# Kernel optimization log

Hardware: AMD Instinct MI355X
Metric: run time of the kernel (lower is better)

Reference implementation:

```python
import jax, jax.numpy as jnp
import numpy as np

D_MODEL = 1024
NUM_HEADS = 16
D_HEAD = D_MODEL // NUM_HEADS
BATCH = 2
SEQ = 2048


def setup_inputs() -> dict:
    key = jax.random.key(0)
    ks = jax.random.split(key, 5)
    std = 0.02
    return {
        "x": jax.random.normal(ks[0], (BATCH, SEQ, D_MODEL), dtype=jnp.float32),
        "Wq": jax.random.normal(ks[1], (D_MODEL, D_MODEL), dtype=jnp.float32) * std,
        "Wk": jax.random.normal(ks[2], (D_MODEL, D_MODEL), dtype=jnp.float32) * std,
        "Wv": jax.random.normal(ks[3], (D_MODEL, D_MODEL), dtype=jnp.float32) * std,
        "Wo": jax.random.normal(ks[4], (D_MODEL, D_MODEL), dtype=jnp.float32) * std,
    }


def reference(x, Wq, Wk, Wv, Wo):
    batch, seq_len, d_model = x.shape
    h, dh = NUM_HEADS, D_HEAD

    def split_heads(W):
        # x @ W.T -> (b, s, d) -> (b, h, s, dh)
        p = jnp.einsum('bsd,ed->bse', x, W)
        return p.reshape(batch, seq_len, h, dh).transpose(0, 2, 1, 3)

    Q = split_heads(Wq)
    K = split_heads(Wk)
    V = split_heads(Wv)

    scale = 1.0 / jnp.sqrt(jnp.asarray(dh, dtype=x.dtype))
    scores = jnp.einsum('bhqd,bhkd->bhqk', Q, K) * scale
    causal = jnp.tril(jnp.ones((seq_len, seq_len), dtype=bool))
    scores = jnp.where(causal, scores, -jnp.inf)
    attn = jax.nn.softmax(scores, axis=-1)
    out = jnp.einsum('bhqk,bhkd->bhqd', attn, V)  # (b, h, s, dh)
    out = out.transpose(0, 2, 1, 3).reshape(batch, seq_len, d_model)
    return jnp.einsum('bsd,ed->bse', out, Wo)
```

## Files before the change

kernel.cpp:

```cpp
#include <hip/hip_runtime.h>

#define D_MODEL 1024
#define NUM_HEADS 16
#define D_HEAD 64
#define BATCH 2
#define SEQ 2048
#define MTOT (BATCH * SEQ)
#define PLANE ((size_t)MTOT * D_MODEL)
#define QSCALE 0.1803368801f

typedef unsigned short us;
typedef __bf16 bf16x8 __attribute__((ext_vector_type(8)));
typedef float floatx4 __attribute__((ext_vector_type(4)));

__device__ __forceinline__ unsigned int f2bf(float f) {
  union { float f; unsigned int i; } v; v.f = f;
  unsigned int r = v.i + 0x7FFFu + ((v.i >> 16) & 1u);
  return r >> 16;
}
__device__ __forceinline__ unsigned int f2bf_tr(float f) {
  union { float f; unsigned int i; } v; v.f = f;
  return v.i >> 16;
}

__global__ __launch_bounds__(256) void convert_all(const float* __restrict__ x,
                                                   const float* __restrict__ Wq,
                                                   const float* __restrict__ Wk,
                                                   const float* __restrict__ Wv,
                                                   const float* __restrict__ Wo,
                                                   us* __restrict__ xbf,
                                                   us* __restrict__ Wqkv,
                                                   us* __restrict__ Wobf) {
  const int i = blockIdx.x * 256 + threadIdx.x;
  const float* src;
  us* dst;
  if (i < (1 << 20)) {
    src = x + (size_t)i * 4;
    dst = xbf + (size_t)i * 4;
  } else {
    const int j = i - (1 << 20);
    const int w = j >> 18;
    const int o = j & ((1 << 18) - 1);
    if (w < 3) {
      const float* ws = (w == 0) ? Wq : (w == 1) ? Wk : Wv;
      src = ws + (size_t)o * 4;
      dst = Wqkv + (size_t)w * (D_MODEL * D_MODEL) + (size_t)o * 4;
    } else {
      src = Wo + (size_t)o * 4;
      dst = Wobf + (size_t)o * 4;
    }
  }
  float4 v = *(const float4*)src;
  uint2 pk;
  pk.x = f2bf(v.x) | (f2bf(v.y) << 16);
  pk.y = f2bf(v.z) | (f2bf(v.w) << 16);
  *(uint2*)dst = pk;
}

template <int CMODE>
__global__ __launch_bounds__(256) void gemm_n64(const us* __restrict__ A,
                                                const us* __restrict__ B,
                                                void* __restrict__ Cv,
                                                int M, int N, int K) {
  __shared__ __bf16 As[2][128 * 32];
  __shared__ __bf16 Bs[2][64 * 32];
  const int tid = threadIdx.x;
  const int wid = tid >> 6;
  const int lane = tid & 63;
  const int bm = blockIdx.y * 128;
  const int bn = blockIdx.x * 64;
  const int wm = wid * 32;
  const int lr = lane & 15;
  const int quad = lane >> 4;

  floatx4 acc[2][4] = {};

  auto stage = [&](int buf, int k0) {
#pragma unroll
    for (int p = 0; p < 2; ++p) {
      const int cb = wid * 128 + p * 64;
      const int c = cb + lane;
      const us* ga = A + (size_t)(bm + (c >> 2)) * K + (k0 + (c & 3) * 8);
      __builtin_amdgcn_global_load_lds((const __attribute__((address_space(1))) void*)ga,
                                       (__attribute__((address_space(3))) void*)(&As[buf][cb * 8]),
                                       16, 0, 0);
    }
    const int cb2 = wid * 64;
    const int c2 = cb2 + lane;
    const us* gb = B + (size_t)(bn + (c2 >> 2)) * K + (k0 + (c2 & 3) * 8);
    __builtin_amdgcn_global_load_lds((const __attribute__((address_space(1))) void*)gb,
                                     (__attribute__((address_space(3))) void*)(&Bs[buf][cb2 * 8]),
                                     16, 0, 0);
  };

  stage(0, 0);
  __syncthreads();

  int cur = 0;
  for (int k0 = 0; k0 < K; k0 += 32) {
    if (k0 + 32 < K) stage(cur ^ 1, k0 + 32);

    bf16x8 a[2], b[4];
#pragma unroll
    for (int i = 0; i < 2; ++i)
      a[i] = *(const bf16x8*)&As[cur][(wm + i * 16 + lr) * 32 + quad * 8];
#pragma unroll
    for (int j = 0; j < 4; ++j)
      b[j] = *(const bf16x8*)&Bs[cur][(j * 16 + lr) * 32 + quad * 8];
#pragma unroll
    for (int i = 0; i < 2; ++i)
#pragma unroll
      for (int j = 0; j < 4; ++j)
        acc[i][j] = __builtin_amdgcn_mfma_f32_16x16x32_bf16(a[i], b[j], acc[i][j], 0, 0, 0);

    __syncthreads();
    cur ^= 1;
  }

#pragma unroll
  for (int i = 0; i < 2; ++i) {
#pragma unroll
    for (int j = 0; j < 4; ++j) {
      const int col = bn + j * 16 + lr;
      if constexpr (CMODE == 1) {
        us* dst = (us*)Cv;
        const int plane = col >> 10;
        if (plane < 2) {
          const float s = (plane == 0) ? QSCALE : 1.0f;
#pragma unroll
          for (int r = 0; r < 4; ++r) {
            const int row = bm + wm + i * 16 + quad * 4 + r;
            dst[(size_t)plane * PLANE + (size_t)row * 1024 + (col & 1023)] =
                (us)f2bf(acc[i][j][r] * s);
          }
        } else {
          const int d = col & 63;
          const int hh = (col >> 6) & 15;
          const int row0 = bm + wm + i * 16 + quad * 4;
          const int bb = row0 >> 11;
          const int ss = row0 & 2047;
          uint2 pk;
          pk.x = f2bf(acc[i][j][0]) | (f2bf(acc[i][j][1]) << 16);
          pk.y = f2bf(acc[i][j][2]) | (f2bf(acc[i][j][3]) << 16);
          *(uint2*)&dst[2 * PLANE + ((size_t)((bb * 16 + hh) * 64 + d)) * 2048 + ss] = pk;
        }
      } else {
#pragma unroll
        for (int r = 0; r < 4; ++r) {
          const int row = bm + wm + i * 16 + quad * 4 + r;
          ((float*)Cv)[(size_t)row * N + col] = acc[i][j][r];
        }
      }
    }
  }
}

#define ASTR 72

__global__ __launch_bounds__(512, 2) void attn_mfma(const us* __restrict__ Qb,
                                                    const us* __restrict__ Kb,
                                                    const us* __restrict__ Vtg,
                                                    us* __restrict__ Ob) {
  const int bx = blockIdx.x;
  const int b = bx >> 8;
  const int idx = bx & 255;
  const int h = idx >> 4;
  const int s0 = idx & 15;
  const int strip = b ? (15 - s0) : s0;
  const int q0 = strip * 128;
  const int ntiles = 2 * strip + 2;
  const int tid = threadIdx.x;
  const int w = tid >> 6;
  const int lane = tid & 63;
  const int lr = lane & 15;
  const int quad = lane >> 4;

  __shared__ us Ks[2][64 * ASTR];
  __shared__ us Vs[2][64 * ASTR];
  __shared__ us Ps[8 * 16 * ASTR];

  const us* kbase = Kb + (size_t)(b * SEQ) * D_MODEL + h * D_HEAD;
  const us* vbase = Vtg + (size_t)((b * 16 + h) * 64) * 2048;
  us* const pg = &Ps[w * 16 * ASTR];

  const int grow = q0 + w * 16;
  const us* qp = Qb + (size_t)(b * SEQ + grow + lr) * D_MODEL + h * D_HEAD;
  const bf16x8 qa0 = *(const bf16x8*)(qp + quad * 8);
  const bf16x8 qa1 = *(const bf16x8*)(qp + 32 + quad * 8);

  floatx4 oacc[4] = {};
  floatx4 lacc = {};
  bf16x8 ones;
#pragma unroll
  for (int i = 0; i < 8; ++i) ones[i] = (__bf16)1.0f;

  const int srow = tid >> 3;
  const int schunk = tid & 7;

  uint4 kreg, vreg;
  kreg = *(const uint4*)(kbase + (size_t)srow * D_MODEL + schunk * 8);
  vreg = *(const uint4*)(vbase + (size_t)srow * 2048 + schunk * 8);
  *(uint4*)&Ks[0][srow * ASTR + schunk * 8] = kreg;
  *(uint4*)&Vs[0][srow * ASTR + schunk * 8] = vreg;
  __syncthreads();

  for (int t = 0; t < ntiles; ++t) {
    const int k0 = t * 64;
    const int cur = t & 1;
    const bool more = (t + 1 < ntiles);

    if (more) {
      const int kn = k0 + 64;
      kreg = *(const uint4*)(kbase + (size_t)(kn + srow) * D_MODEL + schunk * 8);
      vreg = *(const uint4*)(vbase + (size_t)srow * 2048 + kn + schunk * 8);
    }

#pragma unroll
    for (int jt = 0; jt < 4; ++jt) {
      const bf16x8 kb0 = *(const bf16x8*)&Ks[cur][(jt * 16 + lr) * ASTR + quad * 8];
      const bf16x8 kb1 = *(const bf16x8*)&Ks[cur][(jt * 16 + lr) * ASTR + 32 + quad * 8];
      floatx4 s = {};
      s = __builtin_amdgcn_mfma_f32_16x16x32_bf16(kb0, qa0, s, 0, 0, 0);
      s = __builtin_amdgcn_mfma_f32_16x16x32_bf16(kb1, qa1, s, 0, 0, 0);
      const int kb = k0 + jt * 16 + quad * 4;
      const bool needMask = (k0 + jt * 16 + 15 > grow);
      float p[4];
#pragma unroll
      for (int r = 0; r < 4; ++r) {
        float e = __builtin_amdgcn_exp2f(s[r]);
        if (needMask && (kb + r > grow + lr)) e = 0.f;
        p[r] = e;
      }
      uint2 pk;
      pk.x = f2bf_tr(p[0]) | (f2bf_tr(p[1]) << 16);
      pk.y = f2bf_tr(p[2]) | (f2bf_tr(p[3]) << 16);
      *(uint2*)&pg[lr * ASTR + jt * 16 + quad * 4] = pk;
    }

    const bf16x8 pa0 = *(const bf16x8*)&pg[lr * ASTR + quad * 8];
    const bf16x8 pa1 = *(const bf16x8*)&pg[lr * ASTR + 32 + quad * 8];
    lacc = __builtin_amdgcn_mfma_f32_16x16x32_bf16(ones, pa0, lacc, 0, 0, 0);
    lacc = __builtin_amdgcn_mfma_f32_16x16x32_bf16(ones, pa1, lacc, 0, 0, 0);
#pragma unroll
    for (int nt = 0; nt < 4; ++nt) {
      const bf16x8 vb0 = *(const bf16x8*)&Vs[cur][(nt * 16 + lr) * ASTR + quad * 8];
      const bf16x8 vb1 = *(const bf16x8*)&Vs[cur][(nt * 16 + lr) * ASTR + 32 + quad * 8];
      oacc[nt] = __builtin_amdgcn_mfma_f32_16x16x32_bf16(vb0, pa0, oacc[nt], 0, 0, 0);
      oacc[nt] = __builtin_amdgcn_mfma_f32_16x16x32_bf16(vb1, pa1, oacc[nt], 0, 0, 0);
    }

    if (more) {
      const int nxt = cur ^ 1;
      *(uint4*)&Ks[nxt][srow * ASTR + schunk * 8] = kreg;
      *(uint4*)&Vs[nxt][srow * ASTR + schunk * 8] = vreg;
    }
    __syncthreads();
  }

  const float inv = 1.f / lacc[0];
#pragma unroll
  for (int nt = 0; nt < 4; ++nt) {
    uint2 pk;
    pk.x = f2bf_tr(oacc[nt][0] * inv) | (f2bf_tr(oacc[nt][1] * inv) << 16);
    pk.y = f2bf_tr(oacc[nt][2] * inv) | (f2bf_tr(oacc[nt][3] * inv) << 16);
    *(uint2*)&pg[lr * ASTR + nt * 16 + quad * 4] = pk;
  }
#pragma unroll
  for (int p = 0; p < 2; ++p) {
    const int c = lane + 64 * p;
    *(uint4*)(Ob + (size_t)(b * SEQ + grow + (c >> 3)) * D_MODEL + h * D_HEAD + (c & 7) * 8) =
        *(const uint4*)&pg[(c >> 3) * ASTR + (c & 7) * 8];
  }
}

extern "C" void kernel_launch(void* const* d_in, const int* in_sizes, int n_in,
                              void* d_out, int out_size, void* d_ws, size_t ws_size,
                              hipStream_t stream) {
  const float* x  = (const float*)d_in[0];
  const float* Wq = (const float*)d_in[1];
  const float* Wk = (const float*)d_in[2];
  const float* Wv = (const float*)d_in[3];
  const float* Wo = (const float*)d_in[4];

  us* xbf = (us*)d_ws;
  us* Qb  = xbf + PLANE;
  us* Kb  = xbf + 2 * PLANE;
  us* Vt  = xbf + 3 * PLANE;
  us* Wobf = xbf + 4 * PLANE;
  us* Ab  = xbf;
  us* Wqkv = (us*)d_out;
  float* out = (float*)d_out;

  convert_all<<<8192, 256, 0, stream>>>(x, Wq, Wk, Wv, Wo, xbf, Wqkv, Wobf);

  gemm_n64<1><<<dim3(3072 / 64, MTOT / 128), 256, 0, stream>>>(xbf, Wqkv, Qb, MTOT, 3072, D_MODEL);

  attn_mfma<<<512, 512, 0, stream>>>(Qb, Kb, Vt, Ab);

  gemm_n64<2><<<dim3(D_MODEL / 64, MTOT / 128), 256, 0, stream>>>(Ab, Wobf, out, MTOT, D_MODEL, D_MODEL);
}
```

Before: 185.7 us.

## Use 256x256-tile triple-buffered GEMM with direct-to-LDS loads for QKV projection

Replaces the 128x64-tile QKV projection GEMM with a new 512-thread kernel using 256x256 tiles. It adds a three-stage LDS pipeline fed by global_load_lds, an XOR swizzle to avoid bank conflicts, and setprio around the MFMA bursts. The larger tile raises arithmetic intensity and the asynchronous loads are meant to hide memory latency. The grid shrinks to 192 blocks, which may underfill the GPU's 256 CUs, and the kernel needs a large LDS footprint.

```diff
diff --git a/kernel.cpp b/kernel.cpp
--- a/kernel.cpp
+++ b/kernel.cpp
@@ -57,10 +57,135 @@
   *(uint2*)dst = pk;
 }
 
-template <int CMODE>
+__global__ __launch_bounds__(512) void gemm256(const us* __restrict__ A,
+                                               const us* __restrict__ B,
+                                               us* __restrict__ dst,
+                                               int K) {
+  __shared__ us As[3][256 * 32];
+  __shared__ us Bs[3][256 * 32];
+  const int tid = threadIdx.x;
+  const int wid = tid >> 6;
+  const int lane = tid & 63;
+  const int bm = blockIdx.y * 256;
+  const int bn = blockIdx.x * 256;
+  const int wm = (wid >> 2) * 128;
+  const int wn = (wid & 3) * 64;
+  const int lr = lane & 15;
+  const int quad = lane >> 4;
+  const int csel = (quad ^ ((lr >> 1) & 3)) * 8;
+
+  floatx4 acc[8][4] = {};
+
+  const int srow = tid >> 2;
+  const int sc = tid & 3;
+
+  auto stageA = [&](int buf, int k0, int p) {
+    const int row = srow + p * 128;
+    const int cs = (sc ^ ((row >> 1) & 3)) * 8;
+    const us* g = A + (size_t)(bm + row) * K + k0 + cs;
+    __builtin_amdgcn_global_load_lds((const __attribute__((address_space(1))) void*)g,
+                                     (__attribute__((address_space(3))) void*)(&As[buf][row * 32 + sc * 8]),
+                                     16, 0, 0);
+  };
+  auto stageB = [&](int buf, int k0, int p) {
+    const int row = srow + p * 128;
+    const int cs = (sc ^ ((row >> 1) & 3)) * 8;
+    const us* g = B + (size_t)(bn + row) * K + k0 + cs;
+    __builtin_amdgcn_global_load_lds((const __attribute__((address_space(1))) void*)g,
+                                     (__attribute__((address_space(3))) void*)(&Bs[buf][row * 32 + sc * 8]),
+                                     16, 0, 0);
+  };
+
+#pragma unroll
+  for (int p = 0; p < 2; ++p) { stageA(0, 0, p); stageB(0, 0, p); }
+#pragma unroll
+  for (int p = 0; p < 2; ++p) { stageA(1, 32, p); stageB(1, 32, p); }
+  asm volatile("s_waitcnt vmcnt(4)" ::: "memory");
+  asm volatile("s_barrier" ::: "memory");
+
+  const int NT = K >> 5;
+  for (int t = 0; t < NT; ++t) {
+    const int cur = t % 3;
+    const bool pre = (t + 2 < NT);
+    const int nxt = (t + 2) % 3;
+    const int kpre = (t + 2) << 5;
+    const us* Acur = As[cur];
+    const us* Bcur = Bs[cur];
+
+    bf16x8 bfr[4], a[4];
+#pragma unroll
+    for (int j = 0; j < 4; ++j)
+      bfr[j] = *(const bf16x8*)&Bcur[(wn + j * 16 + lr) * 32 + csel];
+#pragma unroll
+    for (int f = 0; f < 4; ++f)
+      a[f] = *(const bf16x8*)&Acur[(wm + f * 16 + lr) * 32 + csel];
+    if (pre) { stageA(nxt, kpre, 0); stageB(nxt, kpre, 0); }
+    asm volatile("s_barrier" ::: "memory");
+    __builtin_amdgcn_s_setprio(1);
+#pragma unroll
+    for (int f = 0; f < 4; ++f)
+#pragma unroll
+      for (int j = 0; j < 4; ++j)
+        acc[f][j] = __builtin_amdgcn_mfma_f32_16x16x32_bf16(a[f], bfr[j], acc[f][j], 0, 0, 0);
+    __builtin_amdgcn_s_setprio(0);
+
+#pragma unroll
+    for (int f = 0; f < 4; ++f)
+      a[f] = *(const bf16x8*)&Acur[(wm + (4 + f) * 16 + lr) * 32 + csel];
+    if (pre) { stageA(nxt, kpre, 1); stageB(nxt, kpre, 1); }
+    asm volatile("s_barrier" ::: "memory");
+    __builtin_amdgcn_s_setprio(1);
+#pragma unroll
+    for (int f = 0; f < 4; ++f)
+#pragma unroll
+      for (int j = 0; j < 4; ++j)
+        acc[4 + f][j] = __builtin_amdgcn_mfma_f32_16x16x32_bf16(a[f], bfr[j], acc[4 + f][j], 0, 0, 0);
+    __builtin_amdgcn_s_setprio(0);
+
+    if (pre) asm volatile("s_waitcnt vmcnt(4)" ::: "memory");
+    else     asm volatile("s_waitcnt vmcnt(0)" ::: "memory");
+    asm volatile("s_barrier" ::: "memory");
+  }
+
+  const int plane = bn >> 10;
+  const int colb = (bn & 1023) + wn;
+  if (plane < 2) {
+    const float s = (plane == 0) ? QSCALE : 1.0f;
+#pragma unroll
+    for (int f = 0; f < 8; ++f) {
+#pragma unroll
+      for (int j = 0; j < 4; ++j) {
+        const int col = colb + j * 16 + lr;
+#pragma unroll
+        for (int r = 0; r < 4; ++r) {
+          const int row = bm + wm + f * 16 + quad * 4 + r;
+          dst[(size_t)plane * PLANE + (size_t)row * 1024 + col] = (us)f2bf(acc[f][j][r] * s);
+        }
+      }
+    }
+  } else {
+#pragma unroll
+    for (int f = 0; f < 8; ++f) {
+#pragma unroll
+      for (int j = 0; j < 4; ++j) {
+        const int cc = colb + j * 16 + lr;
+        const int d = cc & 63;
+        const int hh = cc >> 6;
+        const int row0 = bm + wm + f * 16 + quad * 4;
+        const int bb = row0 >> 11;
+        const int ss = row0 & 2047;
+        uint2 pk;
+        pk.x = f2bf(acc[f][j][0]) | (f2bf(acc[f][j][1]) << 16);
+        pk.y = f2bf(acc[f][j][2]) | (f2bf(acc[f][j][3]) << 16);
+        *(uint2*)&dst[2 * PLANE + ((size_t)((bb * 16 + hh) * 64 + d)) * 2048 + ss] = pk;
+      }
+    }
+  }
+}
+
 __global__ __launch_bounds__(256) void gemm_n64(const us* __restrict__ A,
                                                 const us* __restrict__ B,
-                                                void* __restrict__ Cv,
+                                                float* __restrict__ C,
                                                 int M, int N, int K) {
   __shared__ __bf16 As[2][128 * 32];
   __shared__ __bf16 Bs[2][64 * 32];
@@ -122,34 +247,10 @@
 #pragma unroll
     for (int j = 0; j < 4; ++j) {
       const int col = bn + j * 16 + lr;
-      if constexpr (CMODE == 1) {
-        us* dst = (us*)Cv;
-        const int plane = col >> 10;
-        if (plane < 2) {
-          const float s = (plane == 0) ? QSCALE : 1.0f;
-#pragma unroll
-          for (int r = 0; r < 4; ++r) {
-            const int row = bm + wm + i * 16 + quad * 4 + r;
-            dst[(size_t)plane * PLANE + (size_t)row * 1024 + (col & 1023)] =
-                (us)f2bf(acc[i][j][r] * s);
-          }
-        } else {
-          const int d = col & 63;
-          const int hh = (col >> 6) & 15;
-          const int row0 = bm + wm + i * 16 + quad * 4;
-          const int bb = row0 >> 11;
-          const int ss = row0 & 2047;
-          uint2 pk;
-          pk.x = f2bf(acc[i][j][0]) | (f2bf(acc[i][j][1]) << 16);
-          pk.y = f2bf(acc[i][j][2]) | (f2bf(acc[i][j][3]) << 16);
-          *(uint2*)&dst[2 * PLANE + ((size_t)((bb * 16 + hh) * 64 + d)) * 2048 + ss] = pk;
-        }
-      } else {
-#pragma unroll
-        for (int r = 0; r < 4; ++r) {
-          const int row = bm + wm + i * 16 + quad * 4 + r;
-          ((float*)Cv)[(size_t)row * N + col] = acc[i][j][r];
-        }
+#pragma unroll
+      for (int r = 0; r < 4; ++r) {
+        const int row = bm + wm + i * 16 + quad * 4 + r;
+        C[(size_t)row * N + col] = acc[i][j][r];
       }
     }
   }
@@ -293,9 +394,9 @@
 
   convert_all<<<8192, 256, 0, stream>>>(x, Wq, Wk, Wv, Wo, xbf, Wqkv, Wobf);
 
-  gemm_n64<1><<<dim3(3072 / 64, MTOT / 128), 256, 0, stream>>>(xbf, Wqkv, Qb, MTOT, 3072, D_MODEL);
+  gemm256<<<dim3(3072 / 256, MTOT / 256), 512, 0, stream>>>(xbf, Wqkv, Qb, D_MODEL);
 
   attn_mfma<<<512, 512, 0, stream>>>(Qb, Kb, Vt, Ab);
 
-  gemm_n64<2><<<dim3(D_MODEL / 64, MTOT / 128), 256, 0, stream>>>(Ab, Wobf, out, MTOT, D_MODEL, D_MODEL);
-}
+  gemm_n64<<<dim3(D_MODEL / 64, MTOT / 128), 256, 0, stream>>>(Ab, Wobf, out, MTOT, D_MODEL, D_MODEL);
+}
```

Measured after the change: 178.5 us. 1.04x faster.
